# Kernel tuning notes

Measured on AMD Instinct MI355X. Metric: run time of the kernel, lower is better.

## Reference

```python
import jax, jax.numpy as jnp
import numpy as np

B, C, Q, E, H = 8, 1024, 128, 512, 1024


def setup_inputs() -> dict:
    key = jax.random.key(0)
    ks = jax.random.split(key, 8)
    return {
        "context": jax.random.normal(ks[0], (B, C, E), jnp.float32),
        "question": jax.random.normal(ks[1], (B, Q, E), jnp.float32),
        "context_mask": jnp.ones((B, C), jnp.float32),
        "w_question": jax.random.normal(ks[2], (E,), jnp.float32),
        "w_context": jax.random.normal(ks[3], (E,), jnp.float32),
        "w_multiple": jax.random.normal(ks[4], (E,), jnp.float32),
        "W1": jax.random.normal(ks[5], (4 * E, H), jnp.float32) * 0.02,
        "b1": jnp.zeros((H,), jnp.float32),
        "W2": jax.random.normal(ks[6], (H, 4 * E), jnp.float32) * 0.02,
        "b2": jnp.zeros((4 * E,), jnp.float32),
    }


def reference(context, question, context_mask, w_question, w_context, w_multiple, W1, b1, W2, b2):
    # Dropout is identity at eval time.
    # Trilinear similarity: s[b,c,q] = q.w_q + ctx.w_c + sum_e q_e*ctx_e*w_m_e
    q_w = question @ w_question                                  # (B,Q)
    c_w = context @ w_context                                    # (B,C)
    mult = jnp.einsum("bqe,bce->bcq", question * w_multiple, context)  # avoids (B,C,Q,E)
    sim = q_w[:, None, :] + c_w[:, :, None] + mult               # (B,C,Q)

    # Context2Query: softmax over question dim (dim=2)
    c2q = jnp.einsum("bcq,bqe->bce", jax.nn.softmax(sim, axis=2), question)
    # Query2Context: max over question dim, softmax over context dim (dim=1)
    q2c = jnp.einsum("bc,bce->be", jax.nn.softmax(jnp.max(sim, axis=2), axis=1), context)  # (B,E)

    attended = jnp.concatenate(
        [context, c2q, context * c2q, context * q2c[:, None, :]], axis=2
    )  # (B,C,4E)

    # MaskedLinear: linear then zero out masked context positions
    m = context_mask[:, :, None]
    h = (attended @ W1 + b1) * m
    out = jax.nn.relu((h @ W2 + b2) * m)
    return out
```

## Files before the change

kernel.cpp:

```cpp
#include <hip/hip_runtime.h>

typedef __bf16 bf16;
typedef __bf16 bf16x2 __attribute__((ext_vector_type(2)));
typedef __bf16 bf16x4 __attribute__((ext_vector_type(4)));
typedef __bf16 bf16x8 __attribute__((ext_vector_type(8)));
typedef float f32x4 __attribute__((ext_vector_type(4)));

#define AS1 __attribute__((address_space(1)))
#define AS3 __attribute__((address_space(3)))

__device__ __forceinline__ void async_copy16(const void* g, void* l) {
  __builtin_amdgcn_global_load_lds((const AS1 void*)g, (AS3 void*)l, 16, 0, 0);
}

#define BB 8
#define CC 1024
#define QQ 128
#define EE 512
#define HH 1024
#define FOURE 2048

__global__ __launch_bounds__(256) void prep_kernel(
    const float* __restrict__ W1, const float* __restrict__ W2,
    const float* __restrict__ qst, const float* __restrict__ wmul,
    const float* __restrict__ wqv, bf16* __restrict__ W1T,
    bf16* __restrict__ W2T, bf16* __restrict__ qT,
    bf16* __restrict__ qmh, bf16* __restrict__ qml, float* __restrict__ qw) {
  __shared__ float tile[32][33];
  __shared__ float r4[4];
  int bx = blockIdx.x;
  int t = threadIdx.x;
  if (bx >= 4608) {
    int i = bx - 4608;
    int half = t >> 7, tr = t & 127;
    int rowg = i * 2 + half;
    const float* qrow = qst + (size_t)rowg * EE;
    float4 qv = *(const float4*)&qrow[tr * 4];
    float4 wm4 = *(const float4*)&wmul[tr * 4];
    float4 wq4 = *(const float4*)&wqv[tr * 4];
    float m[4] = {qv.x * wm4.x, qv.y * wm4.y, qv.z * wm4.z, qv.w * wm4.w};
    bf16x4 h, l;
#pragma unroll
    for (int k = 0; k < 4; ++k) {
      bf16 hh = (bf16)m[k];
      h[k] = hh; l[k] = (bf16)(m[k] - (float)hh);
    }
    *(bf16x4*)&qmh[(size_t)rowg * EE + tr * 4] = h;
    *(bf16x4*)&qml[(size_t)rowg * EE + tr * 4] = l;
    float s = qv.x * wq4.x + qv.y * wq4.y + qv.z * wq4.z + qv.w * wq4.w;
#pragma unroll
    for (int off = 32; off; off >>= 1) s += __shfl_xor(s, off);
    if ((t & 63) == 0) r4[t >> 6] = s;
    __syncthreads();
    if (tr == 0) qw[rowg] = r4[half * 2] + r4[half * 2 + 1];
    return;
  }
  const float* src;
  bf16* dst;
  int R, C, idx;
  if (bx < 2048) {
    src = W1; dst = W1T; R = 2048; C = 1024; idx = bx;
  } else if (bx < 4096) {
    src = W2; dst = W2T; R = 1024; C = 2048; idx = bx - 2048;
  } else {
    int i = bx - 4096;
    int b = i >> 6; idx = i & 63;
    src = qst + (size_t)b * QQ * EE; dst = qT + (size_t)b * EE * QQ;
    R = 128; C = 512;
  }
  int ctiles = C >> 5;
  int by = idx / ctiles, cx = idx % ctiles;
  int tx = t & 31, ty = t >> 5;
#pragma unroll
  for (int rr = 0; rr < 4; ++rr)
    tile[ty + rr * 8][tx] = src[(size_t)(by * 32 + ty + rr * 8) * C + cx * 32 + tx];
  __syncthreads();
#pragma unroll
  for (int rr = 0; rr < 4; ++rr)
    dst[(size_t)(cx * 32 + ty + rr * 8) * R + by * 32 + tx] = (bf16)tile[tx][ty + rr * 8];
}

__global__ __launch_bounds__(256) void fused_att_kernel(
    const float* __restrict__ ctx, const bf16* __restrict__ qmh,
    const bf16* __restrict__ qml, const bf16* __restrict__ qT,
    const float* __restrict__ wc, const float* __restrict__ qw,
    float* __restrict__ smax, bf16* __restrict__ att) {
  int b = blockIdx.y;
  int m0 = blockIdx.x * 16;
  __shared__ __align__(16) char U[26880];
  bf16* Ah = (bf16*)(U);
  bf16* Al = (bf16*)(U + 1024);
  bf16* Bh = (bf16*)(U + 2048);
  bf16* Bl = (bf16*)(U + 10240);
  float(*sim_s)[132] = (float(*)[132])(U + 18432);
  bf16* c2q_lds = (bf16*)(U);
  __shared__ float wc_s[EE];
  __shared__ float qw_s[QQ];
  __shared__ float cw_s[16];
  __shared__ bf16 P_lds[16][136];
  int t = threadIdx.x;
  for (int i = t; i < EE; i += 256) wc_s[i] = wc[i];
  if (t < QQ) qw_s[t] = qw[b * QQ + t];
  __syncthreads();
  int wv = t >> 6, ln = t & 63;
  int rl = ln & 15, kq = ln >> 4;
  f32x4 acc[2] = {};
  const float* Ag = ctx + ((size_t)b * CC + m0) * EE;
  const bf16* Bhg = qmh + (size_t)b * QQ * EE;
  const bf16* Blg = qml + (size_t)b * QQ * EE;
  int arow = t >> 4, ae = (t & 15) * 2;
  float cwp = 0.f;
  for (int k0 = 0; k0 < EE; k0 += 32) {
    {
      float2 v = *(const float2*)(Ag + (size_t)arow * EE + k0 + ae);
      cwp += v.x * wc_s[k0 + ae] + v.y * wc_s[k0 + ae + 1];
      bf16 h0 = (bf16)v.x, h1 = (bf16)v.y;
      bf16x2 h, l;
      h[0] = h0; h[1] = h1;
      l[0] = (bf16)(v.x - (float)h0);
      l[1] = (bf16)(v.y - (float)h1);
      int sl = ((ae >> 3) ^ ((arow >> 1) & 3)) * 8 + (ae & 7);
      *(bf16x2*)&Ah[arow * 32 + sl] = h;
      *(bf16x2*)&Al[arow * 32 + sl] = l;
    }
#pragma unroll
    for (int r = 0; r < 2; ++r) {
      int fb = (r * 4 + wv) * 1024 + ln * 16;
      int row = fb >> 6;
      int cq = ((fb >> 4) & 3) ^ ((row >> 1) & 3);
      async_copy16(Bhg + (size_t)row * EE + k0 + cq * 8, (char*)Bh + fb);
      async_copy16(Blg + (size_t)row * EE + k0 + cq * 8, (char*)Bl + fb);
    }
    __syncthreads();
    bf16x8 ah, al, bh[2], bl[2];
    {
      int sl = (kq ^ ((rl >> 1) & 3)) * 8;
      ah = *(const bf16x8*)&Ah[rl * 32 + sl];
      al = *(const bf16x8*)&Al[rl * 32 + sl];
    }
#pragma unroll
    for (int j = 0; j < 2; ++j) {
      int r = wv * 32 + j * 16 + rl;
      int sl = (kq ^ ((r >> 1) & 3)) * 8;
      bh[j] = *(const bf16x8*)&Bh[r * 32 + sl];
      bl[j] = *(const bf16x8*)&Bl[r * 32 + sl];
    }
#pragma unroll
    for (int j = 0; j < 2; ++j) {
      acc[j] = __builtin_amdgcn_mfma_f32_16x16x32_bf16(ah, bh[j], acc[j], 0, 0, 0);
      acc[j] = __builtin_amdgcn_mfma_f32_16x16x32_bf16(ah, bl[j], acc[j], 0, 0, 0);
      acc[j] = __builtin_amdgcn_mfma_f32_16x16x32_bf16(al, bh[j], acc[j], 0, 0, 0);
    }
    __syncthreads();
  }
  {
    float s = cwp;
    s += __shfl_xor(s, 1); s += __shfl_xor(s, 2);
    s += __shfl_xor(s, 4); s += __shfl_xor(s, 8);
    if ((t & 15) == 0) cw_s[arow] = s;
  }
#pragma unroll
  for (int j = 0; j < 2; ++j) {
    int col = wv * 32 + j * 16 + rl;
    float qv = qw_s[col];
    int rbase = kq * 4;
#pragma unroll
    for (int r = 0; r < 4; ++r) sim_s[rbase + r][col] = acc[j][r] + qv;
  }
  __syncthreads();
  {
    int row = t >> 4, cb = t & 15;
    float v[8];
    float mx = -3.4e38f;
#pragma unroll
    for (int k = 0; k < 8; ++k) {
      v[k] = sim_s[row][cb + 16 * k];
      mx = fmaxf(mx, v[k]);
    }
    mx = fmaxf(mx, __shfl_xor(mx, 1));
    mx = fmaxf(mx, __shfl_xor(mx, 2));
    mx = fmaxf(mx, __shfl_xor(mx, 4));
    mx = fmaxf(mx, __shfl_xor(mx, 8));
    float sm = 0.f;
#pragma unroll
    for (int k = 0; k < 8; ++k) { v[k] = __expf(v[k] - mx); sm += v[k]; }
    sm += __shfl_xor(sm, 1);
    sm += __shfl_xor(sm, 2);
    sm += __shfl_xor(sm, 4);
    sm += __shfl_xor(sm, 8);
    float inv = 1.0f / sm;
#pragma unroll
    for (int k = 0; k < 8; ++k) P_lds[row][cb + 16 * k] = (bf16)(v[k] * inv);
    if (cb == 0) smax[b * CC + m0 + row] = mx + cw_s[row];
  }
  __syncthreads();
  f32x4 acc2[8] = {};
  const bf16* qTb = qT + (size_t)b * EE * QQ;
#pragma unroll
  for (int kk = 0; kk < 4; ++kk) {
    bf16x8 af2;
    {
      bf16x4 lo = *(const bf16x4*)&P_lds[rl][kk * 32 + kq * 8];
      bf16x4 hi = *(const bf16x4*)&P_lds[rl][kk * 32 + kq * 8 + 4];
      af2[0] = lo[0]; af2[1] = lo[1]; af2[2] = lo[2]; af2[3] = lo[3];
      af2[4] = hi[0]; af2[5] = hi[1]; af2[6] = hi[2]; af2[7] = hi[3];
    }
#pragma unroll
    for (int j = 0; j < 8; ++j) {
      int n = wv * 128 + j * 16 + rl;
      bf16x8 bfr = *(const bf16x8*)&qTb[(size_t)n * QQ + kk * 32 + kq * 8];
      acc2[j] = __builtin_amdgcn_mfma_f32_16x16x32_bf16(af2, bfr, acc2[j], 0, 0, 0);
    }
  }
#pragma unroll
  for (int j = 0; j < 8; ++j) {
    int col = wv * 128 + j * 16 + rl;
    int rbase = kq * 4;
#pragma unroll
    for (int r = 0; r < 4; ++r)
      c2q_lds[(size_t)(rbase + r) * 520 + col] = (bf16)acc2[j][r];
  }
  __syncthreads();
  {
    int row = t >> 4, tc = t & 15;
    const float* crow = ctx + ((size_t)(b * CC + m0 + row)) * EE;
    bf16* arow_p = att + ((size_t)(b * CC + m0 + row)) * FOURE;
#pragma unroll
    for (int cc = 0; cc < 4; ++cc) {
      int col = cc * 128 + tc * 8;
      bf16x8 q8 = *(const bf16x8*)&c2q_lds[(size_t)row * 520 + col];
      float4 v0 = *(const float4*)&crow[col];
      float4 v1 = *(const float4*)&crow[col + 4];
      float cv[8] = {v0.x, v0.y, v0.z, v0.w, v1.x, v1.y, v1.z, v1.w};
      bf16x8 o0, o2;
#pragma unroll
      for (int k = 0; k < 8; ++k) {
        o0[k] = (bf16)cv[k];
        o2[k] = (bf16)(cv[k] * (float)q8[k]);
      }
      *(bf16x8*)&arow_p[col] = o0;
      *(bf16x8*)&arow_p[EE + col] = q8;
      *(bf16x8*)&arow_p[2 * EE + col] = o2;
    }
  }
}

__global__ __launch_bounds__(256) void q2c_kernel(
    const float* __restrict__ ctx, const float* __restrict__ smax,
    float* __restrict__ q2c) {
  int b = blockIdx.x >> 5, ch = blockIdx.x & 31;
  int t = threadIdx.x;
  __shared__ float red[256];
  __shared__ float w_s[32];
  float v[4];
  float mx = -3.4e38f;
#pragma unroll
  for (int i = 0; i < 4; ++i) {
    v[i] = smax[b * CC + i * 256 + t];
    mx = fmaxf(mx, v[i]);
  }
  red[t] = mx;
  __syncthreads();
  for (int s = 128; s > 0; s >>= 1) {
    if (t < s) red[t] = fmaxf(red[t], red[t + s]);
    __syncthreads();
  }
  mx = red[0];
  __syncthreads();
  float sm = 0.f;
#pragma unroll
  for (int i = 0; i < 4; ++i) sm += __expf(v[i] - mx);
  red[t] = sm;
  __syncthreads();
  for (int s = 128; s > 0; s >>= 1) {
    if (t < s) red[t] += red[t + s];
    __syncthreads();
  }
  float inv = 1.0f / red[0];
  if (t < 32) w_s[t] = __expf(smax[b * CC + ch * 32 + t] - mx) * inv;
  __syncthreads();
  int e = t * 2;
  const float* cb = ctx + ((size_t)b * CC + ch * 32) * EE;
  float a0 = 0.f, a1 = 0.f;
#pragma unroll 8
  for (int r = 0; r < 32; ++r) {
    float2 vv = *(const float2*)&cb[(size_t)r * EE + e];
    float w = w_s[r];
    a0 += w * vv.x;
    a1 += w * vv.y;
  }
  atomicAdd(&q2c[b * EE + e], a0);
  atomicAdd(&q2c[b * EE + e + 1], a1);
}

__global__ __launch_bounds__(256) void att3_kernel(
    const float* __restrict__ ctx, const float* __restrict__ q2c,
    bf16* __restrict__ att) {
  int idx = blockIdx.x * 256 + threadIdx.x;
  int row = idx >> 6;
  int e = (idx & 63) * 8;
  int b = row >> 10;
  float4 v0 = *(const float4*)&ctx[(size_t)row * EE + e];
  float4 v1 = *(const float4*)&ctx[(size_t)row * EE + e + 4];
  float4 g0 = *(const float4*)&q2c[b * EE + e];
  float4 g1 = *(const float4*)&q2c[b * EE + e + 4];
  bf16x8 o;
  o[0] = (bf16)(v0.x * g0.x); o[1] = (bf16)(v0.y * g0.y);
  o[2] = (bf16)(v0.z * g0.z); o[3] = (bf16)(v0.w * g0.w);
  o[4] = (bf16)(v1.x * g1.x); o[5] = (bf16)(v1.y * g1.y);
  o[6] = (bf16)(v1.z * g1.z); o[7] = (bf16)(v1.w * g1.w);
  *(bf16x8*)&att[(size_t)row * FOURE + 3 * EE + e] = o;
}

template <int MT, int OUT_BF16, int RELU, int HAS_BIAS, int HAS_MASK>
__global__ __launch_bounds__(256) void gemm_bt_kernel(
    const bf16* __restrict__ A, const bf16* __restrict__ Bt,
    const float* __restrict__ bias, const float* __restrict__ mask,
    void* __restrict__ Cout, int M, int N, int K, long sA, long sB, long sC) {
  int b = blockIdx.y;
  A += (size_t)b * sA;
  Bt += (size_t)b * sB;
  int ntiles = N >> 7;
  int tiles_per_g = 8 * ntiles;
  int g = blockIdx.x / tiles_per_g, sub = blockIdx.x % tiles_per_g;
  int mt = g * 8 + (sub & 7), ntb = sub >> 3;
  int m0 = mt * MT, n0 = ntb << 7;
  __shared__ bf16 As[MT * 64];
  __shared__ bf16 Bs[128 * 64];
  int t = threadIdx.x, wv = t >> 6, ln = t & 63;
  int wm = wv >> 1, wn = wv & 1;
  constexpr int MI = MT / 32;
  f32x4 acc[MI][4] = {};
  for (int k0 = 0; k0 < K; k0 += 64) {
#pragma unroll
    for (int r = 0; r < MT / 32; ++r) {
      int fb = (r * 4 + wv) * 1024 + ln * 16;
      int row = fb >> 7;
      int q = ((fb >> 4) & 7) ^ (row & 7);
      async_copy16(A + (size_t)(m0 + row) * K + k0 + q * 8,
                   (char*)As + fb);
    }
#pragma unroll
    for (int r = 0; r < 4; ++r) {
      int fb = (r * 4 + wv) * 1024 + ln * 16;
      int row = fb >> 7;
      int q = ((fb >> 4) & 7) ^ (row & 7);
      async_copy16(Bt + (size_t)(n0 + row) * K + k0 + q * 8,
                   (char*)Bs + fb);
    }
    __syncthreads();
    int rl = ln & 15, kq = ln >> 4;
#pragma unroll
    for (int ks = 0; ks < 2; ++ks) {
      int c = ks * 4 + kq;
      bf16x8 af[MI], bfr[4];
#pragma unroll
      for (int i = 0; i < MI; ++i) {
        int row = wm * (MT / 2) + i * 16 + rl;
        af[i] = *(const bf16x8*)&As[row * 64 + ((c ^ (row & 7)) * 8)];
      }
#pragma unroll
      for (int j = 0; j < 4; ++j) {
        int row = wn * 64 + j * 16 + rl;
        bfr[j] = *(const bf16x8*)&Bs[row * 64 + ((c ^ (row & 7)) * 8)];
      }
#pragma unroll
      for (int i = 0; i < MI; ++i)
#pragma unroll
        for (int j = 0; j < 4; ++j)
          acc[i][j] = __builtin_amdgcn_mfma_f32_16x16x32_bf16(af[i], bfr[j], acc[i][j], 0, 0, 0);
    }
    __syncthreads();
  }
  size_t outbase = (size_t)b * sC;
#pragma unroll
  for (int j = 0; j < 4; ++j) {
    int col = n0 + wn * 64 + j * 16 + (ln & 15);
    float bv = HAS_BIAS ? bias[col] : 0.f;
#pragma unroll
    for (int i = 0; i < MI; ++i) {
      int rbase = m0 + wm * (MT / 2) + i * 16 + ((ln >> 4) << 2);
#pragma unroll
      for (int r = 0; r < 4; ++r) {
        int row = rbase + r;
        float v = acc[i][j][r] + bv;
        if (HAS_MASK) v *= mask[row];
        if (RELU) v = fmaxf(v, 0.f);
        if (OUT_BF16)
          ((bf16*)Cout)[outbase + (size_t)row * N + col] = (bf16)v;
        else
          ((float*)Cout)[outbase + (size_t)row * N + col] = v;
      }
    }
  }
}

extern "C" void kernel_launch(void* const* d_in, const int* in_sizes, int n_in,
                              void* d_out, int out_size, void* d_ws, size_t ws_size,
                              hipStream_t stream) {
  const float* ctx = (const float*)d_in[0];
  const float* qst = (const float*)d_in[1];
  const float* mask = (const float*)d_in[2];
  const float* wqv = (const float*)d_in[3];
  const float* wcv = (const float*)d_in[4];
  const float* wmul = (const float*)d_in[5];
  const float* W1 = (const float*)d_in[6];
  const float* b1 = (const float*)d_in[7];
  const float* W2 = (const float*)d_in[8];
  const float* b2 = (const float*)d_in[9];
  float* out = (float*)d_out;
  char* ws = (char*)d_ws;

  bf16* att = (bf16*)(ws);
  bf16* hbuf = (bf16*)(ws + 33554432);
  bf16* W1T = (bf16*)(ws + 50331648);
  bf16* W2T = (bf16*)(ws + 54525952);
  bf16* qT = (bf16*)(ws + 58720256);
  bf16* qmh = (bf16*)(ws + 59768832);
  bf16* qml = (bf16*)(ws + 60817408);
  float* smax = (float*)(ws + 61865984);
  float* q2c = (float*)(ws + 61898752);
  float* qw = (float*)(ws + 61915136);

  prep_kernel<<<5120, 256, 0, stream>>>(W1, W2, qst, wmul, wqv,
                                        W1T, W2T, qT, qmh, qml, qw);
  fused_att_kernel<<<dim3(64, BB), 256, 0, stream>>>(ctx, qmh, qml, qT, wcv,
                                                     qw, smax, att);
  hipMemsetAsync(q2c, 0, BB * EE * sizeof(float), stream);
  q2c_kernel<<<256, 256, 0, stream>>>(ctx, smax, q2c);
  att3_kernel<<<2048, 256, 0, stream>>>(ctx, q2c, att);
  gemm_bt_kernel<128, 1, 0, 1, 1><<<dim3(512, 1), 256, 0, stream>>>(
      att, W1T, b1, mask, hbuf, 8192, 1024, 2048, 0, 0, 0);
  gemm_bt_kernel<128, 0, 1, 1, 1><<<dim3(1024, 1), 256, 0, stream>>>(
      hbuf, W2T, b2, mask, out, 8192, 2048, 1024, 0, 0, 0);
}
```

Before: 229.2 us.

## Load MFMA operands directly from global memory, dropping LDS staging and barriers

```diff
diff --git a/kernel.cpp b/kernel.cpp
--- a/kernel.cpp
+++ b/kernel.cpp
@@ -87,82 +87,56 @@
     float* __restrict__ smax, bf16* __restrict__ att) {
   int b = blockIdx.y;
   int m0 = blockIdx.x * 16;
-  __shared__ __align__(16) char U[26880];
-  bf16* Ah = (bf16*)(U);
-  bf16* Al = (bf16*)(U + 1024);
-  bf16* Bh = (bf16*)(U + 2048);
-  bf16* Bl = (bf16*)(U + 10240);
-  float(*sim_s)[132] = (float(*)[132])(U + 18432);
+  __shared__ __align__(16) char U[16640];
+  float(*sim_s)[132] = (float(*)[132])(U);
   bf16* c2q_lds = (bf16*)(U);
-  __shared__ float wc_s[EE];
-  __shared__ float qw_s[QQ];
+  __shared__ bf16 P_lds[16][136];
   __shared__ float cw_s[16];
-  __shared__ bf16 P_lds[16][136];
   int t = threadIdx.x;
-  for (int i = t; i < EE; i += 256) wc_s[i] = wc[i];
-  if (t < QQ) qw_s[t] = qw[b * QQ + t];
-  __syncthreads();
   int wv = t >> 6, ln = t & 63;
   int rl = ln & 15, kq = ln >> 4;
   f32x4 acc[2] = {};
-  const float* Ag = ctx + ((size_t)b * CC + m0) * EE;
-  const bf16* Bhg = qmh + (size_t)b * QQ * EE;
-  const bf16* Blg = qml + (size_t)b * QQ * EE;
-  int arow = t >> 4, ae = (t & 15) * 2;
+  const float* Arow = ctx + ((size_t)(b * CC + m0 + rl)) * EE;
+  const bf16* Bh0 = qmh + ((size_t)(b * QQ + wv * 32 + rl)) * EE;
+  const bf16* Bh1 = Bh0 + 16 * EE;
+  const bf16* Bl0 = qml + ((size_t)(b * QQ + wv * 32 + rl)) * EE;
+  const bf16* Bl1 = Bl0 + 16 * EE;
   float cwp = 0.f;
+#pragma unroll
   for (int k0 = 0; k0 < EE; k0 += 32) {
-    {
-      float2 v = *(const float2*)(Ag + (size_t)arow * EE + k0 + ae);
-      cwp += v.x * wc_s[k0 + ae] + v.y * wc_s[k0 + ae + 1];
-      bf16 h0 = (bf16)v.x, h1 = (bf16)v.y;
-      bf16x2 h, l;
-      h[0] = h0; h[1] = h1;
-      l[0] = (bf16)(v.x - (float)h0);
-      l[1] = (bf16)(v.y - (float)h1);
-      int sl = ((ae >> 3) ^ ((arow >> 1) & 3)) * 8 + (ae & 7);
-      *(bf16x2*)&Ah[arow * 32 + sl] = h;
-      *(bf16x2*)&Al[arow * 32 + sl] = l;
-    }
-#pragma unroll
-    for (int r = 0; r < 2; ++r) {
-      int fb = (r * 4 + wv) * 1024 + ln * 16;
-      int row = fb >> 6;
-      int cq = ((fb >> 4) & 3) ^ ((row >> 1) & 3);
-      async_copy16(Bhg + (size_t)row * EE + k0 + cq * 8, (char*)Bh + fb);
-      async_copy16(Blg + (size_t)row * EE + k0 + cq * 8, (char*)Bl + fb);
-    }
-    __syncthreads();
-    bf16x8 ah, al, bh[2], bl[2];
-    {
-      int sl = (kq ^ ((rl >> 1) & 3)) * 8;
-      ah = *(const bf16x8*)&Ah[rl * 32 + sl];
-      al = *(const bf16x8*)&Al[rl * 32 + sl];
-    }
-#pragma unroll
-    for (int j = 0; j < 2; ++j) {
-      int r = wv * 32 + j * 16 + rl;
-      int sl = (kq ^ ((r >> 1) & 3)) * 8;
-      bh[j] = *(const bf16x8*)&Bh[r * 32 + sl];
-      bl[j] = *(const bf16x8*)&Bl[r * 32 + sl];
-    }
+    int ko = k0 + kq * 8;
+    float4 a0 = *(const float4*)(Arow + ko);
+    float4 a1 = *(const float4*)(Arow + ko + 4);
+    float4 w0 = *(const float4*)(wc + ko);
+    float4 w1 = *(const float4*)(wc + ko + 4);
+    cwp += a0.x * w0.x + a0.y * w0.y + a0.z * w0.z + a0.w * w0.w +
+           a1.x * w1.x + a1.y * w1.y + a1.z * w1.z + a1.w * w1.w;
+    float av[8] = {a0.x, a0.y, a0.z, a0.w, a1.x, a1.y, a1.z, a1.w};
+    bf16x8 ah, al;
+#pragma unroll
+    for (int i = 0; i < 8; ++i) {
+      bf16 hh = (bf16)av[i];
+      ah[i] = hh; al[i] = (bf16)(av[i] - (float)hh);
+    }
+    bf16x8 bh[2], bl[2];
+    bh[0] = *(const bf16x8*)(Bh0 + ko);
+    bh[1] = *(const bf16x8*)(Bh1 + ko);
+    bl[0] = *(const bf16x8*)(Bl0 + ko);
+    bl[1] = *(const bf16x8*)(Bl1 + ko);
 #pragma unroll
     for (int j = 0; j < 2; ++j) {
       acc[j] = __builtin_amdgcn_mfma_f32_16x16x32_bf16(ah, bh[j], acc[j], 0, 0, 0);
       acc[j] = __builtin_amdgcn_mfma_f32_16x16x32_bf16(ah, bl[j], acc[j], 0, 0, 0);
       acc[j] = __builtin_amdgcn_mfma_f32_16x16x32_bf16(al, bh[j], acc[j], 0, 0, 0);
     }
-    __syncthreads();
-  }
-  {
-    float s = cwp;
-    s += __shfl_xor(s, 1); s += __shfl_xor(s, 2);
-    s += __shfl_xor(s, 4); s += __shfl_xor(s, 8);
-    if ((t & 15) == 0) cw_s[arow] = s;
-  }
+  }
+  cwp += __shfl_xor(cwp, 16);
+  cwp += __shfl_xor(cwp, 32);
+  if (t < 16) cw_s[t] = cwp;
 #pragma unroll
   for (int j = 0; j < 2; ++j) {
     int col = wv * 32 + j * 16 + rl;
-    float qv = qw_s[col];
+    float qv = qw[b * QQ + col];
     int rbase = kq * 4;
 #pragma unroll
     for (int r = 0; r < 4; ++r) sim_s[rbase + r][col] = acc[j][r] + qv;
```

New measurement: 236.8 us. 3.3% more time.
